# Optimization experiments

Measured on AMD Instinct MI355X. Metric: run time of the kernel, lower is better.

## Reference

```python
import jax, jax.numpy as jnp
import numpy as np
from jax import lax

N, CIN, H, W = 128, 1024, 14, 14
CF, TH = 128, 128          # cv_filter, te_hidden
HP, GT, FP, A = 256, 256, 256, 32


def setup_inputs() -> dict:
    key = jax.random.key(0)
    ks = jax.random.split(key, 12)
    s = 0.05
    return {
        "image": jax.random.normal(ks[0], (N, CIN, H, W), jnp.float32),
        "code": jax.random.normal(ks[1], (N, TH), jnp.float32),
        "conv_w": jax.random.normal(ks[2], (CF, CIN, 3, 3), jnp.float32) * 0.02,
        "conv_b": jnp.zeros((CF,), jnp.float32),
        "hp_w0": jax.random.normal(ks[3], (CF + 2 + TH, HP), jnp.float32) * s,
        "hp_b0": jnp.zeros((HP,), jnp.float32),
        "hp_w1": jax.random.normal(ks[4], (HP, 1), jnp.float32) * s,
        "hp_b1": jnp.zeros((1,), jnp.float32),
        "gt_w0": jax.random.normal(ks[5], ((CF + 2) * 2 + TH, GT), jnp.float32) * s,
        "gt_b0": jnp.zeros((GT,), jnp.float32),
        "gt_w1": jax.random.normal(ks[6], (GT, GT), jnp.float32) * s,
        "gt_b1": jnp.zeros((GT,), jnp.float32),
        "fp_w0": jax.random.normal(ks[7], (GT, FP), jnp.float32) * s,
        "fp_b0": jnp.zeros((FP,), jnp.float32),
        "fp_w1": jax.random.normal(ks[8], (FP, A), jnp.float32) * s,
        "fp_b1": jnp.zeros((A,), jnp.float32),
    }


def _sarn(image, code, conv_w, conv_b, hp_w0, hp_b0, hp_w1, hp_b1,
          gt_w0, gt_b0, gt_w1, gt_b1, fp_w0, fp_b0, fp_w1, fp_b1):
    # visual_resize: 3x3 conv, stride 1, pad 1 (NCHW)
    x = lax.conv_general_dilated(image, conv_w, (1, 1), "SAME",
                                 dimension_numbers=("NCHW", "OIHW", "NCHW"))
    x = x + conv_b[None, :, None, None]                       # [n, cf, h, w]
    n, c, h, w = x.shape
    o = h * w
    # sarn_encode: append x/y coordinate channels and question code
    xc = jnp.broadcast_to(jnp.linspace(-1.0, 1.0, h).reshape(1, 1, h, 1), (n, 1, h, w))
    yc = jnp.broadcast_to(jnp.linspace(-1.0, 1.0, w).reshape(1, 1, 1, w), (n, 1, h, w))
    coord = jnp.concatenate([x, xc, yc], axis=1)              # [n, cf+2, h, w]
    q = jnp.broadcast_to(code[:, :, None, None], (n, code.shape[1], h, w))
    qenc = jnp.concatenate([coord, q], axis=1)                # [n, cf+2+th, h, w]
    ce = coord.reshape(n, c + 2, o).transpose(0, 2, 1)        # [n, o, cf+2]
    qe = qenc.reshape(n, -1, o).transpose(0, 2, 1)            # [n, o, cf+2+th]
    # h_psi: per-object attention logit
    a = jax.nn.relu(jnp.einsum("nod,dh->noh", qe, hp_w0) + hp_b0)
    att = jnp.einsum("noh,hk->nok", a, hp_w1) + hp_b1         # [n, o, 1]
    # sarn_pair: softmax select a single soft object, pair with every object
    sel = jax.nn.softmax(att[..., 0], axis=1)                 # [n, o]
    selected = jnp.einsum("no,nod->nd", sel, ce)              # [n, cf+2]
    pairs = jnp.concatenate(
        [qe, jnp.broadcast_to(selected[:, None, :], ce.shape)], axis=2)  # [n, o, 2*(cf+2)+th]
    # g_theta MLP + sum over objects
    g = jax.nn.relu(jnp.einsum("nop,pg->nog", pairs, gt_w0) + gt_b0)
    g = jax.nn.relu(jnp.einsum("nog,gk->nok", g, gt_w1) + gt_b1)
    relations = g.sum(axis=1)                                 # [n, gt]
    # f_phi MLP -> answer logits
    f = jax.nn.relu(relations @ fp_w0 + fp_b0)
    return f @ fp_w1 + fp_b1                                  # [n, a_size]


def reference(image, code, conv_w, conv_b, hp_w0, hp_b0, hp_w1, hp_b1,
              gt_w0, gt_b0, gt_w1, gt_b1, fp_w0, fp_b0, fp_w1, fp_b1):
    return _sarn(image, code, conv_w, conv_b, hp_w0, hp_b0, hp_w1, hp_b1,
                 gt_w0, gt_b0, gt_w1, gt_b1, fp_w0, fp_b0, fp_w1, fp_b1)
```

## Files before the change

### kernel.cpp

```cpp
#include <hip/hip_runtime.h>
#include <stdint.h>

typedef unsigned short u16;
typedef __bf16 bf16x8 __attribute__((ext_vector_type(8)));
typedef float f32x4 __attribute__((ext_vector_type(4)));

__device__ __forceinline__ u16 f2b(float f) {
  union { float f; uint32_t u; } v; v.f = f;
  uint32_t r = v.u + 0x7fffu + ((v.u >> 16) & 1u);
  return (u16)(r >> 16);
}
__device__ __forceinline__ float b2f(u16 b) {
  union { float f; uint32_t u; } v; v.u = ((uint32_t)b) << 16;
  return v.f;
}
__device__ __forceinline__ void g2l16(const void* g, void* l) {
  __builtin_amdgcn_global_load_lds(
      (const __attribute__((address_space(1))) void*)g,
      (__attribute__((address_space(3))) void*)l, 16, 0, 0);
}

#define N_SAMP 128
#define OPAD   224
#define ROWS   (N_SAMP * OPAD)

__global__ __launch_bounds__(256) void prep_weights(
    const float* __restrict__ conv_w, const float* __restrict__ hp_w0,
    const float* __restrict__ gt_w0, const float* __restrict__ gt_w1,
    u16* __restrict__ W2, u16* __restrict__ hp_w0t,
    u16* __restrict__ gt_w0t, u16* __restrict__ gt_w1t) {
  int idx = blockIdx.x * 256 + threadIdx.x;
  const int nW2 = 9 * 128 * 1024;
  const int nHP = 256 * 288;
  const int nGT0 = 256 * 288;
  const int nGT1 = 256 * 256;
  if (idx < nW2) {
    int s = idx / 131072; int r = idx & 131071;
    int cf = r >> 10; int cin = r & 1023;
    W2[idx] = f2b(conv_w[(cf * 1024 + cin) * 9 + s]);
    return;
  }
  idx -= nW2;
  if (idx < nHP) {
    int nn = idx / 288, kk = idx % 288;
    hp_w0t[nn * 288 + kk] = (kk < 258) ? f2b(hp_w0[kk * 256 + nn]) : (u16)0;
    return;
  }
  idx -= nHP;
  if (idx < nGT0) {
    int nn = idx / 288, kk = idx % 288;
    gt_w0t[nn * 288 + kk] = (kk < 258) ? f2b(gt_w0[kk * 256 + nn]) : (u16)0;
    return;
  }
  idx -= nGT0;
  if (idx < nGT1) {
    int nn = idx >> 8, kk = idx & 255;
    gt_w1t[nn * 256 + kk] = f2b(gt_w1[kk * 256 + nn]);
  }
}

__global__ __launch_bounds__(256) void prep_img(const float* __restrict__ image,
                                                u16* __restrict__ imgT) {
  __shared__ float t[64][197];
  int n = blockIdx.x >> 4;
  int cin0 = (blockIdx.x & 15) * 64;
  const float* src = image + ((size_t)n * 1024 + cin0) * 196;
  for (int e = threadIdx.x; e < 64 * 196; e += 256) {
    int c = e / 196, sp = e % 196;
    t[c][sp] = src[c * 196 + sp];
  }
  __syncthreads();
  int w = threadIdx.x >> 6, lane = threadIdx.x & 63;
  for (int i = 0; i < 64; ++i) {
    int spg = i * 4 + w;
    int gy = spg >> 4, gx = spg & 15;
    float v = 0.f;
    if (gy >= 1 && gy <= 14 && gx >= 1 && gx <= 14) v = t[lane][(gy - 1) * 14 + (gx - 1)];
    imgT[(((size_t)(n * 256 + spg)) << 10) + cin0 + lane] = f2b(v);
  }
}

__global__ __launch_bounds__(256) void fill_qe(const float* __restrict__ code,
                                               u16* __restrict__ qeb) {
  int base = blockIdx.x * 8;
  for (int rr = 0; rr < 8; ++rr) {
    int r = base + rr;
    int n = r / 224, o = r % 224;
    int y = o / 14, x = o % 14;
    bool valid = o < 196;
    u16* row = qeb + (size_t)r * 288;
    for (int c = threadIdx.x; c < 288; c += 256) {
      u16 v;
      if (c < 128) { if (valid) continue; v = 0; }
      else if (c == 128) v = valid ? f2b(-1.f + 2.f * y / 13.f) : (u16)0;
      else if (c == 129) v = valid ? f2b(-1.f + 2.f * x / 13.f) : (u16)0;
      else if (c < 258) v = valid ? f2b(code[n * 128 + (c - 130)]) : (u16)0;
      else v = 0;
      row[c] = v;
    }
  }
}

__global__ __launch_bounds__(256) void conv_gemm(
    const u16* __restrict__ imgT, const u16* __restrict__ W2,
    float* __restrict__ convAcc) {
  __shared__ __align__(16) u16 lA[112 * 64];
  __shared__ __align__(16) u16 lB[128 * 64];
  int tid = threadIdx.x, lane = tid & 63, w = tid >> 6;
  int wg = blockIdx.x;
  int xcd = wg & 7, grp = wg >> 3;
  int n = ((grp / 6) << 3) | xcd;
  int r6 = grp % 6;
  int oh = r6 / 3, ks = r6 % 3;
  int oBase = oh * 112;
  size_t nBase = (size_t)n << 8;
  int rowIn = lane >> 3;
  int cA = ((lane & 7) ^ rowIn) << 3;

  int yxA[4];
  for (int ii = 0; ii < 4; ++ii) {
    int t = w + ii * 4;
    int o = oBase + t * 8 + rowIn;
    bool valid = o < 196;
    int y = o / 14, x = o - y * 14;
    yxA[ii] = valid ? (y * 16 + x) : 0;
  }

  f32x4 acc[7][2];
#pragma unroll
  for (int mt = 0; mt < 7; ++mt)
#pragma unroll
    for (int j = 0; j < 2; ++j) acc[mt][j] = (f32x4){0.f, 0.f, 0.f, 0.f};

  int l = lane & 15, q = lane >> 4;
  for (int si = 0; si < 3; ++si) {
    int s = ks * 3 + si;
    int off = (s / 3) * 16 + (s % 3);
    const u16* Ws = W2 + ((size_t)(s * 128) << 10);
    for (int cb = 0; cb < 16; ++cb) {
      int k0 = cb << 6;
      __syncthreads();
      g2l16(imgT + ((nBase + (size_t)(yxA[0] + off)) << 10) + k0 + cA, &lA[(w) * 512]);
      g2l16(imgT + ((nBase + (size_t)(yxA[1] + off)) << 10) + k0 + cA, &lA[(w + 4) * 512]);
      g2l16(imgT + ((nBase + (size_t)(yxA[2] + off)) << 10) + k0 + cA, &lA[(w + 8) * 512]);
      if (w < 2)
        g2l16(imgT + ((nBase + (size_t)(yxA[3] + off)) << 10) + k0 + cA, &lA[(w + 12) * 512]);
#pragma unroll
      for (int ii = 0; ii < 4; ++ii) {
        int t = w + ii * 4;
        g2l16(Ws + ((size_t)(t * 8 + rowIn) << 10) + k0 + cA, &lB[t * 512]);
      }
      __syncthreads();
#pragma unroll
      for (int kk = 0; kk < 2; ++kk) {
        int co = ((((kk << 2) | q) ^ (l & 7)) << 3);
        bf16x8 af[7];
#pragma unroll
        for (int mt = 0; mt < 7; ++mt)
          af[mt] = *(const bf16x8*)&lA[(mt * 16 + l) * 64 + co];
#pragma unroll
        for (int jj = 0; jj < 2; ++jj) {
          bf16x8 bb = *(const bf16x8*)&lB[(w * 32 + jj * 16 + l) * 64 + co];
#pragma unroll
          for (int mt = 0; mt < 7; ++mt)
            acc[mt][jj] = __builtin_amdgcn_mfma_f32_16x16x32_bf16(af[mt], bb, acc[mt][jj], 0, 0, 0);
        }
      }
    }
  }
#pragma unroll
  for (int mt = 0; mt < 7; ++mt) {
    int o = oBase + mt * 16 + q * 4;
#pragma unroll
    for (int r4 = 0; r4 < 4; ++r4) {
      if (o + r4 < 196) {
        float* dst = convAcc + (size_t)(n * 224 + o + r4) * 128 + w * 32 + l;
        atomicAdd(dst, acc[mt][0][r4]);
        atomicAdd(dst + 16, acc[mt][1][r4]);
      }
    }
  }
}

__global__ __launch_bounds__(256) void conv_fix(
    const float* __restrict__ convAcc, const float* __restrict__ conv_b,
    u16* __restrict__ qeb) {
  int idx = blockIdx.x * 256 + threadIdx.x;
  int row196 = idx >> 5;
  int c0 = (idx & 31) << 2;
  int n = row196 / 196, o = row196 - n * 196;
  size_t row = (size_t)(n * 224 + o);
  const float4 v = *(const float4*)(convAcc + (row << 7) + c0);
  const float4 b = *(const float4*)(conv_b + c0);
  ushort4 pk;
  pk.x = f2b(v.x + b.x); pk.y = f2b(v.y + b.y);
  pk.z = f2b(v.z + b.z); pk.w = f2b(v.w + b.w);
  *(ushort4*)(qeb + row * 288 + c0) = pk;
}

template <int MODE, int KP, int KC>
__global__ __launch_bounds__(256) void gemm_kernel(
    const u16* __restrict__ A, const u16* __restrict__ Bt,
    const float* __restrict__ bias, const float* __restrict__ vec,
    float* __restrict__ outF, u16* __restrict__ outB) {
  __shared__ __align__(16) u16 lA[112 * 32];
  __shared__ __align__(16) u16 lB[128 * 32];
  int tid = threadIdx.x, lane = tid & 63, w = tid >> 6;
  int bx = blockIdx.x, by = blockIdx.y;
  int r0 = bx * 112;
  int cBase = by * 128;
  int kb = (((lane & 3) ^ ((lane >> 3) & 3)) << 3);
  int rA0 = r0 + w * 16 + (lane >> 2);
  int rA1 = r0 + (w + 4) * 16 + (lane >> 2);
  bool has1 = (w < 3);
  const u16* gA0 = A + (size_t)rA0 * KP + kb;
  const u16* gA1 = A + (size_t)rA1 * KP + kb;
  int cB0 = cBase + w * 16 + (lane >> 2);
  int cB1 = cBase + (w + 4) * 16 + (lane >> 2);
  const u16* gB0 = Bt + (size_t)cB0 * KP + kb;
  const u16* gB1 = Bt + (size_t)cB1 * KP + kb;

  f32x4 acc[7][2];
#pragma unroll
  for (int mt = 0; mt < 7; ++mt)
#pragma unroll
    for (int j = 0; j < 2; ++j) acc[mt][j] = (f32x4){0.f, 0.f, 0.f, 0.f};
  int colW = w * 32;
  int l = lane & 15, q = lane >> 4;
  int co = ((q ^ ((l >> 1) & 3)) << 3);

  for (int cb = 0; cb < KC; ++cb) {
    __syncthreads();
    g2l16(gA0 + cb * 32, &lA[w * 512]);
    if (has1) g2l16(gA1 + cb * 32, &lA[(w + 4) * 512]);
    g2l16(gB0 + cb * 32, &lB[w * 512]);
    g2l16(gB1 + cb * 32, &lB[(w + 4) * 512]);
    __syncthreads();
    bf16x8 af[7];
#pragma unroll
    for (int mt = 0; mt < 7; ++mt)
      af[mt] = *(const bf16x8*)&lA[(mt * 16 + l) * 32 + co];
#pragma unroll
    for (int j = 0; j < 2; ++j) {
      bf16x8 bfr = *(const bf16x8*)&lB[(colW + j * 16 + l) * 32 + co];
#pragma unroll
      for (int mt = 0; mt < 7; ++mt)
        acc[mt][j] = __builtin_amdgcn_mfma_f32_16x16x32_bf16(af[mt], bfr, acc[mt][j], 0, 0, 0);
    }
  }

  int q4 = lane >> 4, c = lane & 15;
  if (MODE == 0) {
    float attp[7][4];
#pragma unroll
    for (int mt = 0; mt < 7; ++mt)
#pragma unroll
      for (int r = 0; r < 4; ++r) attp[mt][r] = 0.f;
#pragma unroll
    for (int j = 0; j < 2; ++j) {
      int col = cBase + colW + j * 16 + c;
      float b0 = bias[col], w1 = vec[col];
#pragma unroll
      for (int mt = 0; mt < 7; ++mt)
#pragma unroll
        for (int r = 0; r < 4; ++r) {
          float v = fmaxf(acc[mt][j][r] + b0, 0.f);
          attp[mt][r] += v * w1;
        }
    }
#pragma unroll
    for (int mt = 0; mt < 7; ++mt)
#pragma unroll
      for (int r = 0; r < 4; ++r) {
        float p = attp[mt][r];
        p += __shfl_xor(p, 1, 64);
        p += __shfl_xor(p, 2, 64);
        p += __shfl_xor(p, 4, 64);
        p += __shfl_xor(p, 8, 64);
        if (c == 0) atomicAdd(&outF[r0 + mt * 16 + q4 * 4 + r], p);
      }
  } else if (MODE == 1) {
    int n = bx >> 1;
#pragma unroll
    for (int mt = 0; mt < 7; ++mt)
#pragma unroll
      for (int j = 0; j < 2; ++j) {
        int col = cBase + colW + j * 16 + c;
        float b = bias[n * 256 + col];
#pragma unroll
        for (int r = 0; r < 4; ++r) {
          int row = r0 + mt * 16 + q4 * 4 + r;
          outB[(size_t)row * 256 + col] = f2b(fmaxf(acc[mt][j][r] + b, 0.f));
        }
      }
  } else {
    int n = bx >> 1;
    int ob = (bx & 1) * 112;
#pragma unroll
    for (int j = 0; j < 2; ++j) {
      int col = cBase + colW + j * 16 + c;
      float b = bias[col];
      float sum = 0.f;
#pragma unroll
      for (int mt = 0; mt < 7; ++mt)
#pragma unroll
        for (int r = 0; r < 4; ++r) {
          int o = ob + mt * 16 + q4 * 4 + r;
          if (o < 196) sum += fmaxf(acc[mt][j][r] + b, 0.f);
        }
      sum += __shfl_xor(sum, 16, 64);
      sum += __shfl_xor(sum, 32, 64);
      if (q4 == 0) atomicAdd(&outF[n * 256 + col], sum);
    }
  }
}

__global__ __launch_bounds__(256) void sel_kernel(
    const float* __restrict__ att, const u16* __restrict__ qeb,
    const float* __restrict__ gt_w0, const float* __restrict__ gt_b0,
    float* __restrict__ bias2) {
  int n = blockIdx.x, t = threadIdx.x;
  int w = t >> 6, lane = t & 63;
  __shared__ u16 sq[196][130];
  __shared__ float sm[196];
  __shared__ float sel[130];
  __shared__ float red[8];
  const u16* base = qeb + (size_t)n * 224 * 288;
  for (int o = w; o < 196; o += 4) {
    const u16* rowp = base + (size_t)o * 288;
    for (int c = lane; c < 130; c += 64) sq[o][c] = rowp[c];
  }
  float a = (t < 196) ? att[n * 224 + t] : -1e30f;
  float m = a;
  for (int mask = 1; mask < 64; mask <<= 1) m = fmaxf(m, __shfl_xor(m, mask, 64));
  if (lane == 0) red[w] = m;
  __syncthreads();
  float M = fmaxf(fmaxf(red[0], red[1]), fmaxf(red[2], red[3]));
  float e = (t < 196) ? expf(a - M) : 0.f;
  float sAcc = e;
  for (int mask = 1; mask < 64; mask <<= 1) sAcc += __shfl_xor(sAcc, mask, 64);
  if (lane == 0) red[4 + w] = sAcc;
  __syncthreads();
  float S = red[4] + red[5] + red[6] + red[7];
  if (t < 196) sm[t] = e / S;
  __syncthreads();
  if (t < 130) {
    float acc = 0.f;
    for (int o = 0; o < 196; ++o) acc += sm[o] * b2f(sq[o][t]);
    sel[t] = acc;
  }
  __syncthreads();
  float acc2 = gt_b0[t];
  for (int d = 0; d < 130; ++d) acc2 += sel[d] * gt_w0[(258 + d) * 256 + t];
  bias2[n * 256 + t] = acc2;
}

__global__ __launch_bounds__(256) void fphi(
    const float* __restrict__ relations, const float* __restrict__ fp_w0,
    const float* __restrict__ fp_b0, const float* __restrict__ fp_w1,
    const float* __restrict__ fp_b1, float* __restrict__ out) {
  int n = blockIdx.x, t = threadIdx.x;
  __shared__ float rel[256];
  __shared__ float f[256];
  rel[t] = relations[n * 256 + t];
  __syncthreads();
  float acc = fp_b0[t];
  for (int k = 0; k < 256; ++k) acc += rel[k] * fp_w0[k * 256 + t];
  f[t] = fmaxf(acc, 0.f);
  __syncthreads();
  if (t < 32) {
    float o = fp_b1[0];
    for (int k = 0; k < 256; ++k) o += f[k] * fp_w1[k * 32 + t];
    out[n * 32 + t] = o;
  }
}

extern "C" void kernel_launch(void* const* d_in, const int* in_sizes, int n_in,
                              void* d_out, int out_size, void* d_ws, size_t ws_size,
                              hipStream_t stream) {
  const float* image = (const float*)d_in[0];
  const float* code = (const float*)d_in[1];
  const float* conv_w = (const float*)d_in[2];
  const float* conv_b = (const float*)d_in[3];
  const float* hp_w0 = (const float*)d_in[4];
  const float* hp_b0 = (const float*)d_in[5];
  const float* hp_w1 = (const float*)d_in[6];
  const float* gt_w0 = (const float*)d_in[8];
  const float* gt_b0 = (const float*)d_in[9];
  const float* gt_w1 = (const float*)d_in[10];
  const float* gt_b1 = (const float*)d_in[11];
  const float* fp_w0 = (const float*)d_in[12];
  const float* fp_b0 = (const float*)d_in[13];
  const float* fp_w1 = (const float*)d_in[14];
  const float* fp_b1 = (const float*)d_in[15];
  float* out = (float*)d_out;

  char* p = (char*)d_ws;
  u16* imgT = (u16*)p;   p += (size_t)128 * 256 * 1024 * 2;
  u16* W2 = (u16*)p;     p += (size_t)9 * 128 * 1024 * 2;
  u16* qeb = (u16*)p;    p += (size_t)ROWS * 288 * 2;
  u16* hp_w0t = (u16*)p; p += (size_t)256 * 288 * 2;
  u16* gt_w0t = (u16*)p; p += (size_t)256 * 288 * 2;
  u16* gt_w1t = (u16*)p; p += (size_t)256 * 256 * 2;
  float* att = (float*)p;   p += (size_t)ROWS * 4;
  float* bias2 = (float*)p; p += (size_t)128 * 256 * 4;
  float* convAcc = (float*)p; p += (size_t)ROWS * 128 * 4;
  float* relations = (float*)p; p += (size_t)128 * 256 * 4;
  u16* g1 = (u16*)convAcc;

  hipMemsetAsync(att, 0, (size_t)ROWS * 4, stream);
  hipMemsetAsync(relations, 0, (size_t)128 * 256 * 4, stream);
  hipMemsetAsync(convAcc, 0, (size_t)ROWS * 128 * 4, stream);

  prep_weights<<<5440, 256, 0, stream>>>(conv_w, hp_w0, gt_w0, gt_w1, W2, hp_w0t, gt_w0t, gt_w1t);
  prep_img<<<2048, 256, 0, stream>>>(image, imgT);
  fill_qe<<<ROWS / 8, 256, 0, stream>>>(code, qeb);
  conv_gemm<<<768, 256, 0, stream>>>(imgT, W2, convAcc);
  conv_fix<<<3136, 256, 0, stream>>>(convAcc, conv_b, qeb);
  gemm_kernel<0, 288, 9><<<dim3(256, 2), 256, 0, stream>>>(qeb, hp_w0t, hp_b0, hp_w1, att, nullptr);
  sel_kernel<<<128, 256, 0, stream>>>(att, qeb, gt_w0, gt_b0, bias2);
  gemm_kernel<1, 288, 9><<<dim3(256, 2), 256, 0, stream>>>(qeb, gt_w0t, bias2, nullptr, nullptr, g1);
  gemm_kernel<2, 256, 8><<<dim3(256, 2), 256, 0, stream>>>(g1, gt_w1t, gt_b1, nullptr, relations, nullptr);
  fphi<<<128, 256, 0, stream>>>(relations, fp_w0, fp_b0, fp_w1, fp_b1, out);
}
```

Baseline: 415.8 us.

## Double-buffer LDS tiles in conv and MLP GEMMs to overlap loads with MFMA

Converts the conv_gemm and gemm_kernel main loops to a two-stage LDS ping-pong pipeline. The next K-chunk is prefetched with global_load_lds while the current one is computed, using partial vmcnt waits and raw s_barrier plus sched_barrier in place of two __syncthreads per iteration. The goal is to hide global load latency behind the MFMAs. LDS use doubles, which may lower occupancy, and A tiles are padded to 128 rows so every wave issues the same number of loads, with the extra rows reading a clamped address.

```diff
diff --git a/kernel.cpp b/kernel.cpp
--- a/kernel.cpp
+++ b/kernel.cpp
@@ -104,8 +104,8 @@
 __global__ __launch_bounds__(256) void conv_gemm(
     const u16* __restrict__ imgT, const u16* __restrict__ W2,
     float* __restrict__ convAcc) {
-  __shared__ __align__(16) u16 lA[112 * 64];
-  __shared__ __align__(16) u16 lB[128 * 64];
+  __shared__ __align__(16) u16 lA[2][128 * 64];
+  __shared__ __align__(16) u16 lB[2][128 * 64];
   int tid = threadIdx.x, lane = tid & 63, w = tid >> 6;
   int wg = blockIdx.x;
   int xcd = wg & 7, grp = wg >> 3;
@@ -121,7 +121,7 @@
   for (int ii = 0; ii < 4; ++ii) {
     int t = w + ii * 4;
     int o = oBase + t * 8 + rowIn;
-    bool valid = o < 196;
+    bool valid = (o < 196) && (t < 14);
     int y = o / 14, x = o - y * 14;
     yxA[ii] = valid ? (y * 16 + x) : 0;
   }
@@ -133,41 +133,56 @@
     for (int j = 0; j < 2; ++j) acc[mt][j] = (f32x4){0.f, 0.f, 0.f, 0.f};
 
   int l = lane & 15, q = lane >> 4;
-  for (int si = 0; si < 3; ++si) {
-    int s = ks * 3 + si;
-    int off = (s / 3) * 16 + (s % 3);
-    const u16* Ws = W2 + ((size_t)(s * 128) << 10);
-    for (int cb = 0; cb < 16; ++cb) {
-      int k0 = cb << 6;
-      __syncthreads();
-      g2l16(imgT + ((nBase + (size_t)(yxA[0] + off)) << 10) + k0 + cA, &lA[(w) * 512]);
-      g2l16(imgT + ((nBase + (size_t)(yxA[1] + off)) << 10) + k0 + cA, &lA[(w + 4) * 512]);
-      g2l16(imgT + ((nBase + (size_t)(yxA[2] + off)) << 10) + k0 + cA, &lA[(w + 8) * 512]);
-      if (w < 2)
-        g2l16(imgT + ((nBase + (size_t)(yxA[3] + off)) << 10) + k0 + cA, &lA[(w + 12) * 512]);
-#pragma unroll
-      for (int ii = 0; ii < 4; ++ii) {
-        int t = w + ii * 4;
-        g2l16(Ws + ((size_t)(t * 8 + rowIn) << 10) + k0 + cA, &lB[t * 512]);
+
+  auto STAGE = [&](int buf, int si, int k0) {
+    int off = ks * 16 + si;
+    const u16* Ws = W2 + ((size_t)((ks * 3 + si) * 128) << 10);
+#pragma unroll
+    for (int ii = 0; ii < 4; ++ii)
+      g2l16(imgT + ((nBase + (size_t)(yxA[ii] + off)) << 10) + k0 + cA,
+            &lA[buf][(w + ii * 4) * 512]);
+#pragma unroll
+    for (int ii = 0; ii < 4; ++ii)
+      g2l16(Ws + ((size_t)((w + ii * 4) * 8 + rowIn) << 10) + k0 + cA,
+            &lB[buf][(w + ii * 4) * 512]);
+  };
+
+  auto COMPUTE = [&](int cur) {
+#pragma unroll
+    for (int kk = 0; kk < 2; ++kk) {
+      int co = ((((kk << 2) | q) ^ (l & 7)) << 3);
+      bf16x8 af[7];
+#pragma unroll
+      for (int mt = 0; mt < 7; ++mt)
+        af[mt] = *(const bf16x8*)&lA[cur][(mt * 16 + l) * 64 + co];
+#pragma unroll
+      for (int jj = 0; jj < 2; ++jj) {
+        bf16x8 bb = *(const bf16x8*)&lB[cur][(w * 32 + jj * 16 + l) * 64 + co];
+#pragma unroll
+        for (int mt = 0; mt < 7; ++mt)
+          acc[mt][jj] = __builtin_amdgcn_mfma_f32_16x16x32_bf16(af[mt], bb, acc[mt][jj], 0, 0, 0);
       }
-      __syncthreads();
-#pragma unroll
-      for (int kk = 0; kk < 2; ++kk) {
-        int co = ((((kk << 2) | q) ^ (l & 7)) << 3);
-        bf16x8 af[7];
-#pragma unroll
-        for (int mt = 0; mt < 7; ++mt)
-          af[mt] = *(const bf16x8*)&lA[(mt * 16 + l) * 64 + co];
-#pragma unroll
-        for (int jj = 0; jj < 2; ++jj) {
-          bf16x8 bb = *(const bf16x8*)&lB[(w * 32 + jj * 16 + l) * 64 + co];
-#pragma unroll
-          for (int mt = 0; mt < 7; ++mt)
-            acc[mt][jj] = __builtin_amdgcn_mfma_f32_16x16x32_bf16(af[mt], bb, acc[mt][jj], 0, 0, 0);
-        }
-      }
-    }
-  }
+    }
+  };
+
+  STAGE(0, 0, 0);
+#pragma unroll 2
+  for (int it = 0; it < 47; ++it) {
+    int nxt = it + 1;
+    STAGE(nxt & 1, nxt >> 4, (nxt & 15) << 6);
+    asm volatile("s_waitcnt vmcnt(8)" ::: "memory");
+    __builtin_amdgcn_s_barrier();
+    __builtin_amdgcn_sched_barrier(0);
+    COMPUTE(it & 1);
+    __builtin_amdgcn_sched_barrier(0);
+    __builtin_amdgcn_s_barrier();
+    __builtin_amdgcn_sched_barrier(0);
+  }
+  asm volatile("s_waitcnt vmcnt(0)" ::: "memory");
+  __builtin_amdgcn_s_barrier();
+  __builtin_amdgcn_sched_barrier(0);
+  COMPUTE(1);
+
 #pragma unroll
   for (int mt = 0; mt < 7; ++mt) {
     int o = oBase + mt * 16 + q * 4;
@@ -203,8 +218,8 @@
     const u16* __restrict__ A, const u16* __restrict__ Bt,
     const float* __restrict__ bias, const float* __restrict__ vec,
     float* __restrict__ outF, u16* __restrict__ outB) {
-  __shared__ __align__(16) u16 lA[112 * 32];
-  __shared__ __align__(16) u16 lB[128 * 32];
+  __shared__ __align__(16) u16 lA[2][128 * 32];
+  __shared__ __align__(16) u16 lB[2][128 * 32];
   int tid = threadIdx.x, lane = tid & 63, w = tid >> 6;
   int bx = blockIdx.x, by = blockIdx.y;
   int r0 = bx * 112;
@@ -212,7 +227,6 @@
   int kb = (((lane & 3) ^ ((lane >> 3) & 3)) << 3);
   int rA0 = r0 + w * 16 + (lane >> 2);
   int rA1 = r0 + (w + 4) * 16 + (lane >> 2);
-  bool has1 = (w < 3);
   const u16* gA0 = A + (size_t)rA0 * KP + kb;
   const u16* gA1 = A + (size_t)rA1 * KP + kb;
   int cB0 = cBase + w * 16 + (lane >> 2);
@@ -229,25 +243,43 @@
   int l = lane & 15, q = lane >> 4;
   int co = ((q ^ ((l >> 1) & 3)) << 3);
 
-  for (int cb = 0; cb < KC; ++cb) {
-    __syncthreads();
-    g2l16(gA0 + cb * 32, &lA[w * 512]);
-    if (has1) g2l16(gA1 + cb * 32, &lA[(w + 4) * 512]);
-    g2l16(gB0 + cb * 32, &lB[w * 512]);
-    g2l16(gB1 + cb * 32, &lB[(w + 4) * 512]);
-    __syncthreads();
+  auto STAGE = [&](int buf, int cb) {
+    g2l16(gA0 + cb * 32, &lA[buf][w * 512]);
+    g2l16(gA1 + cb * 32, &lA[buf][(w + 4) * 512]);
+    g2l16(gB0 + cb * 32, &lB[buf][w * 512]);
+    g2l16(gB1 + cb * 32, &lB[buf][(w + 4) * 512]);
+  };
+
+  auto COMPUTE = [&](int cur) {
     bf16x8 af[7];
 #pragma unroll
     for (int mt = 0; mt < 7; ++mt)
-      af[mt] = *(const bf16x8*)&lA[(mt * 16 + l) * 32 + co];
+      af[mt] = *(const bf16x8*)&lA[cur][(mt * 16 + l) * 32 + co];
 #pragma unroll
     for (int j = 0; j < 2; ++j) {
-      bf16x8 bfr = *(const bf16x8*)&lB[(colW + j * 16 + l) * 32 + co];
+      bf16x8 bfr = *(const bf16x8*)&lB[cur][(colW + j * 16 + l) * 32 + co];
 #pragma unroll
       for (int mt = 0; mt < 7; ++mt)
         acc[mt][j] = __builtin_amdgcn_mfma_f32_16x16x32_bf16(af[mt], bfr, acc[mt][j], 0, 0, 0);
     }
-  }
+  };
+
+  STAGE(0, 0);
+#pragma unroll
+  for (int it = 0; it < KC - 1; ++it) {
+    STAGE((it & 1) ^ 1, it + 1);
+    asm volatile("s_waitcnt vmcnt(4)" ::: "memory");
+    __builtin_amdgcn_s_barrier();
+    __builtin_amdgcn_sched_barrier(0);
+    COMPUTE(it & 1);
+    __builtin_amdgcn_sched_barrier(0);
+    __builtin_amdgcn_s_barrier();
+    __builtin_amdgcn_sched_barrier(0);
+  }
+  asm volatile("s_waitcnt vmcnt(0)" ::: "memory");
+  __builtin_amdgcn_s_barrier();
+  __builtin_amdgcn_sched_barrier(0);
+  COMPUTE((KC - 1) & 1);
 
   int q4 = lane >> 4, c = lane & 15;
   if (MODE == 0) {
```

Result: slower. 425.7 us (+2.4%).

## Fold per-sample code projection into biases and double-buffer GEMM loads

Applied to the files above, without the earlier changes.

The question code is constant across objects, so its contribution to the hp and g_theta first layers is computed once per sample and folded into per-sample bias vectors. This shrinks the qe row width from 288 to 160 and the K loop of both first-layer GEMMs from 9 to 5 chunks, and shrinks fill_qe as well. The GEMM kernel also gains double-buffered LDS staging with explicit waitcnt and barriers so loads overlap compute. The cost is some extra scalar work in prep_weights and sel_kernel, and the A tile now loads a 128-row block (the 112-row tile plus 16 rows beyond it) instead of exactly 112.

```diff
diff --git a/kernel.cpp b/kernel.cpp
--- a/kernel.cpp
+++ b/kernel.cpp
@@ -23,16 +23,19 @@
 #define N_SAMP 128
 #define OPAD   224
 #define ROWS   (N_SAMP * OPAD)
+#define KQ     160
 
 __global__ __launch_bounds__(256) void prep_weights(
     const float* __restrict__ conv_w, const float* __restrict__ hp_w0,
     const float* __restrict__ gt_w0, const float* __restrict__ gt_w1,
+    const float* __restrict__ hp_b0, const float* __restrict__ code,
     u16* __restrict__ W2, u16* __restrict__ hp_w0t,
-    u16* __restrict__ gt_w0t, u16* __restrict__ gt_w1t) {
+    u16* __restrict__ gt_w0t, u16* __restrict__ gt_w1t,
+    float* __restrict__ biasHP) {
   int idx = blockIdx.x * 256 + threadIdx.x;
   const int nW2 = 9 * 128 * 1024;
-  const int nHP = 256 * 288;
-  const int nGT0 = 256 * 288;
+  const int nHP = 256 * KQ;
+  const int nGT0 = 256 * KQ;
   const int nGT1 = 256 * 256;
   if (idx < nW2) {
     int s = idx / 131072; int r = idx & 131071;
@@ -42,20 +45,29 @@
   }
   idx -= nW2;
   if (idx < nHP) {
-    int nn = idx / 288, kk = idx % 288;
-    hp_w0t[nn * 288 + kk] = (kk < 258) ? f2b(hp_w0[kk * 256 + nn]) : (u16)0;
+    int nn = idx / KQ, kk = idx % KQ;
+    hp_w0t[nn * KQ + kk] = (kk < 130) ? f2b(hp_w0[kk * 256 + nn]) : (u16)0;
     return;
   }
   idx -= nHP;
   if (idx < nGT0) {
-    int nn = idx / 288, kk = idx % 288;
-    gt_w0t[nn * 288 + kk] = (kk < 258) ? f2b(gt_w0[kk * 256 + nn]) : (u16)0;
+    int nn = idx / KQ, kk = idx % KQ;
+    gt_w0t[nn * KQ + kk] = (kk < 130) ? f2b(gt_w0[kk * 256 + nn]) : (u16)0;
     return;
   }
   idx -= nGT0;
   if (idx < nGT1) {
     int nn = idx >> 8, kk = idx & 255;
     gt_w1t[nn * 256 + kk] = f2b(gt_w1[kk * 256 + nn]);
+    return;
+  }
+  idx -= nGT1;
+  {
+    int n = idx >> 8, t = idx & 255;
+    float acc = hp_b0[t];
+    for (int d = 0; d < 128; ++d)
+      acc += code[n * 128 + d] * hp_w0[(130 + d) * 256 + t];
+    biasHP[n * 256 + t] = acc;
   }
 }
 
@@ -80,25 +92,24 @@
   }
 }
 
-__global__ __launch_bounds__(256) void fill_qe(const float* __restrict__ code,
-                                               u16* __restrict__ qeb) {
-  int base = blockIdx.x * 8;
-  for (int rr = 0; rr < 8; ++rr) {
-    int r = base + rr;
-    int n = r / 224, o = r % 224;
-    int y = o / 14, x = o % 14;
-    bool valid = o < 196;
-    u16* row = qeb + (size_t)r * 288;
-    for (int c = threadIdx.x; c < 288; c += 256) {
-      u16 v;
-      if (c < 128) { if (valid) continue; v = 0; }
-      else if (c == 128) v = valid ? f2b(-1.f + 2.f * y / 13.f) : (u16)0;
-      else if (c == 129) v = valid ? f2b(-1.f + 2.f * x / 13.f) : (u16)0;
-      else if (c < 258) v = valid ? f2b(code[n * 128 + (c - 130)]) : (u16)0;
-      else v = 0;
-      row[c] = v;
-    }
-  }
+__global__ __launch_bounds__(256) void fill_qe(u16* __restrict__ qeb) {
+  int idx = blockIdx.x * 256 + threadIdx.x;
+  if (idx < ROWS * 8) {
+    int row = idx >> 3, qd = idx & 7;
+    int o = row % 224;
+    ushort4 v = {0, 0, 0, 0};
+    if (o < 196 && qd == 0) {
+      int y = o / 14, x = o % 14;
+      v.x = f2b(-1.f + 2.f * y / 13.f);
+      v.y = f2b(-1.f + 2.f * x / 13.f);
+    }
+    *(ushort4*)(qeb + (size_t)row * KQ + 128 + qd * 4) = v;
+    return;
+  }
+  idx -= ROWS * 8;
+  int pr = idx >> 5, qd = idx & 31;
+  int row = (pr / 28) * 224 + 196 + (pr % 28);
+  *(ushort4*)(qeb + (size_t)row * KQ + qd * 4) = (ushort4){0, 0, 0, 0};
 }
 
 __global__ __launch_bounds__(256) void conv_gemm(
@@ -195,7 +206,7 @@
   ushort4 pk;
   pk.x = f2b(v.x + b.x); pk.y = f2b(v.y + b.y);
   pk.z = f2b(v.z + b.z); pk.w = f2b(v.w + b.w);
-  *(ushort4*)(qeb + row * 288 + c0) = pk;
+  *(ushort4*)(qeb + row * KQ + c0) = pk;
 }
 
 template <int MODE, int KP, int KC>
@@ -203,8 +214,8 @@
     const u16* __restrict__ A, const u16* __restrict__ Bt,
     const float* __restrict__ bias, const float* __restrict__ vec,
     float* __restrict__ outF, u16* __restrict__ outB) {
-  __shared__ __align__(16) u16 lA[112 * 32];
-  __shared__ __align__(16) u16 lB[128 * 32];
+  __shared__ __align__(16) u16 lA[2][128 * 32];
+  __shared__ __align__(16) u16 lB[2][128 * 32];
   int tid = threadIdx.x, lane = tid & 63, w = tid >> 6;
   int bx = blockIdx.x, by = blockIdx.y;
   int r0 = bx * 112;
@@ -212,7 +223,6 @@
   int kb = (((lane & 3) ^ ((lane >> 3) & 3)) << 3);
   int rA0 = r0 + w * 16 + (lane >> 2);
   int rA1 = r0 + (w + 4) * 16 + (lane >> 2);
-  bool has1 = (w < 3);
   const u16* gA0 = A + (size_t)rA0 * KP + kb;
   const u16* gA1 = A + (size_t)rA1 * KP + kb;
   int cB0 = cBase + w * 16 + (lane >> 2);
@@ -229,28 +239,46 @@
   int l = lane & 15, q = lane >> 4;
   int co = ((q ^ ((l >> 1) & 3)) << 3);
 
-  for (int cb = 0; cb < KC; ++cb) {
-    __syncthreads();
-    g2l16(gA0 + cb * 32, &lA[w * 512]);
-    if (has1) g2l16(gA1 + cb * 32, &lA[(w + 4) * 512]);
-    g2l16(gB0 + cb * 32, &lB[w * 512]);
-    g2l16(gB1 + cb * 32, &lB[(w + 4) * 512]);
-    __syncthreads();
+  auto STAGE = [&](int buf, int cb) {
+    g2l16(gA0 + cb * 32, &lA[buf][w * 512]);
+    g2l16(gA1 + cb * 32, &lA[buf][(w + 4) * 512]);
+    g2l16(gB0 + cb * 32, &lB[buf][w * 512]);
+    g2l16(gB1 + cb * 32, &lB[buf][(w + 4) * 512]);
+  };
+
+  auto COMPUTE = [&](int cur) {
     bf16x8 af[7];
 #pragma unroll
     for (int mt = 0; mt < 7; ++mt)
-      af[mt] = *(const bf16x8*)&lA[(mt * 16 + l) * 32 + co];
+      af[mt] = *(const bf16x8*)&lA[cur][(mt * 16 + l) * 32 + co];
 #pragma unroll
     for (int j = 0; j < 2; ++j) {
-      bf16x8 bfr = *(const bf16x8*)&lB[(colW + j * 16 + l) * 32 + co];
+      bf16x8 bfr = *(const bf16x8*)&lB[cur][(colW + j * 16 + l) * 32 + co];
 #pragma unroll
       for (int mt = 0; mt < 7; ++mt)
         acc[mt][j] = __builtin_amdgcn_mfma_f32_16x16x32_bf16(af[mt], bfr, acc[mt][j], 0, 0, 0);
     }
-  }
+  };
+
+  STAGE(0, 0);
+#pragma unroll
+  for (int it = 0; it < KC - 1; ++it) {
+    STAGE((it & 1) ^ 1, it + 1);
+    asm volatile("s_waitcnt vmcnt(4)" ::: "memory");
+    __builtin_amdgcn_s_barrier();
+    __builtin_amdgcn_sched_barrier(0);
+    COMPUTE(it & 1);
+    __builtin_amdgcn_s_barrier();
+    __builtin_amdgcn_sched_barrier(0);
+  }
+  asm volatile("s_waitcnt vmcnt(0)" ::: "memory");
+  __builtin_amdgcn_s_barrier();
+  __builtin_amdgcn_sched_barrier(0);
+  COMPUTE((KC - 1) & 1);
 
   int q4 = lane >> 4, c = lane & 15;
   if (MODE == 0) {
+    int n = bx >> 1;
     float attp[7][4];
 #pragma unroll
     for (int mt = 0; mt < 7; ++mt)
@@ -259,7 +287,7 @@
 #pragma unroll
     for (int j = 0; j < 2; ++j) {
       int col = cBase + colW + j * 16 + c;
-      float b0 = bias[col], w1 = vec[col];
+      float b0 = bias[n * 256 + col], w1 = vec[col];
 #pragma unroll
       for (int mt = 0; mt < 7; ++mt)
 #pragma unroll
@@ -318,16 +346,16 @@
 __global__ __launch_bounds__(256) void sel_kernel(
     const float* __restrict__ att, const u16* __restrict__ qeb,
     const float* __restrict__ gt_w0, const float* __restrict__ gt_b0,
-    float* __restrict__ bias2) {
+    const float* __restrict__ code, float* __restrict__ bias2) {
   int n = blockIdx.x, t = threadIdx.x;
   int w = t >> 6, lane = t & 63;
   __shared__ u16 sq[196][130];
   __shared__ float sm[196];
   __shared__ float sel[130];
   __shared__ float red[8];
-  const u16* base = qeb + (size_t)n * 224 * 288;
+  const u16* base = qeb + (size_t)n * 224 * KQ;
   for (int o = w; o < 196; o += 4) {
-    const u16* rowp = base + (size_t)o * 288;
+    const u16* rowp = base + (size_t)o * KQ;
     for (int c = lane; c < 130; c += 64) sq[o][c] = rowp[c];
   }
   float a = (t < 196) ? att[n * 224 + t] : -1e30f;
@@ -352,6 +380,7 @@
   __syncthreads();
   float acc2 = gt_b0[t];
   for (int d = 0; d < 130; ++d) acc2 += sel[d] * gt_w0[(258 + d) * 256 + t];
+  for (int d = 0; d < 128; ++d) acc2 += code[n * 128 + d] * gt_w0[(130 + d) * 256 + t];
   bias2[n * 256 + t] = acc2;
 }
 
@@ -398,12 +427,13 @@
   char* p = (char*)d_ws;
   u16* imgT = (u16*)p;   p += (size_t)128 * 256 * 1024 * 2;
   u16* W2 = (u16*)p;     p += (size_t)9 * 128 * 1024 * 2;
-  u16* qeb = (u16*)p;    p += (size_t)ROWS * 288 * 2;
-  u16* hp_w0t = (u16*)p; p += (size_t)256 * 288 * 2;
-  u16* gt_w0t = (u16*)p; p += (size_t)256 * 288 * 2;
+  u16* qeb = (u16*)p;    p += (size_t)ROWS * KQ * 2;
+  u16* hp_w0t = (u16*)p; p += (size_t)256 * KQ * 2;
+  u16* gt_w0t = (u16*)p; p += (size_t)256 * KQ * 2;
   u16* gt_w1t = (u16*)p; p += (size_t)256 * 256 * 2;
-  float* att = (float*)p;   p += (size_t)ROWS * 4;
-  float* bias2 = (float*)p; p += (size_t)128 * 256 * 4;
+  float* att = (float*)p;    p += (size_t)ROWS * 4;
+  float* bias2 = (float*)p;  p += (size_t)128 * 256 * 4;
+  float* biasHP = (float*)p; p += (size_t)128 * 256 * 4;
   float* convAcc = (float*)p; p += (size_t)ROWS * 128 * 4;
   float* relations = (float*)p; p += (size_t)128 * 256 * 4;
   u16* g1 = (u16*)convAcc;
@@ -412,14 +442,15 @@
   hipMemsetAsync(relations, 0, (size_t)128 * 256 * 4, stream);
   hipMemsetAsync(convAcc, 0, (size_t)ROWS * 128 * 4, stream);
 
-  prep_weights<<<5440, 256, 0, stream>>>(conv_w, hp_w0, gt_w0, gt_w1, W2, hp_w0t, gt_w0t, gt_w1t);
+  prep_weights<<<5312, 256, 0, stream>>>(conv_w, hp_w0, gt_w0, gt_w1, hp_b0, code,
+                                         W2, hp_w0t, gt_w0t, gt_w1t, biasHP);
   prep_img<<<2048, 256, 0, stream>>>(image, imgT);
-  fill_qe<<<ROWS / 8, 256, 0, stream>>>(code, qeb);
+  fill_qe<<<1344, 256, 0, stream>>>(qeb);
   conv_gemm<<<768, 256, 0, stream>>>(imgT, W2, convAcc);
   conv_fix<<<3136, 256, 0, stream>>>(convAcc, conv_b, qeb);
-  gemm_kernel<0, 288, 9><<<dim3(256, 2), 256, 0, stream>>>(qeb, hp_w0t, hp_b0, hp_w1, att, nullptr);
-  sel_kernel<<<128, 256, 0, stream>>>(att, qeb, gt_w0, gt_b0, bias2);
-  gemm_kernel<1, 288, 9><<<dim3(256, 2), 256, 0, stream>>>(qeb, gt_w0t, bias2, nullptr, nullptr, g1);
+  gemm_kernel<0, KQ, 5><<<dim3(256, 2), 256, 0, stream>>>(qeb, hp_w0t, biasHP, hp_w1, att, nullptr);
+  sel_kernel<<<128, 256, 0, stream>>>(att, qeb, gt_w0, gt_b0, code, bias2);
+  gemm_kernel<1, KQ, 5><<<dim3(256, 2), 256, 0, stream>>>(qeb, gt_w0t, bias2, nullptr, nullptr, g1);
   gemm_kernel<2, 256, 8><<<dim3(256, 2), 256, 0, stream>>>(g1, gt_w1t, gt_b1, nullptr, relations, nullptr);
   fphi<<<128, 256, 0, stream>>>(relations, fp_w0, fp_b0, fp_w1, fp_b1, out);
 }
```

After: 397.0 us. 1.05x faster.
